# Performance work log

Measured on AMD Instinct MI355X. Metric: run time of the kernel, lower is better.

The kernel has to match this reference:

```python
import jax, jax.numpy as jnp
import numpy as np

H, KV, D, HID = 32, 2, 128, 4096
SQ, SMAX, CP, L = 1024, 4096, 3072, 4
LAYER_IDX = 0


def setup_inputs() -> dict:
    key = jax.random.key(0)
    ks = jax.random.split(key, 14)
    hidden_states = jax.random.normal(ks[0], (1, HID, 1, SQ), jnp.float32)
    # RoPE tables (values in [-1,1]; layout per forward: cos/sin act on last dim of K,
    # cos_t/sin_t are the transposed tables acting on dim -2 of Q)
    cos = jax.random.uniform(ks[1], (1, 1, SQ, D), jnp.float32, -1.0, 1.0)
    sin = jax.random.uniform(ks[2], (1, 1, SQ, D), jnp.float32, -1.0, 1.0)
    cos_t = jax.random.uniform(ks[3], (1, 1, D, SQ), jnp.float32, -1.0, 1.0)
    sin_t = jax.random.uniform(ks[4], (1, 1, D, SQ), jnp.float32, -1.0, 1.0)
    # causal mask in (kv_pos, q_pos) layout: query q sits at absolute position CP+q
    kv_pos = jnp.arange(SMAX)[:, None]
    q_pos = jnp.arange(SQ)[None, :]
    attention_mask = jnp.where(kv_pos <= CP + q_pos, 0.0, -1e9).astype(jnp.float32)[None, None]
    key_cache = jax.random.normal(ks[5], (L, KV, SMAX, D), jnp.float32)
    value_cache = jax.random.normal(ks[6], (L, KV, SMAX, D), jnp.float32)
    s = 0.02
    wq = jax.random.normal(ks[7], (H * D, HID), jnp.float32) * s
    bq = jax.random.normal(ks[8], (H * D,), jnp.float32) * s
    wk = jax.random.normal(ks[9], (KV * D, HID), jnp.float32) * s
    bk = jax.random.normal(ks[10], (KV * D,), jnp.float32) * s
    wv = jax.random.normal(ks[11], (KV * D, HID), jnp.float32) * s
    bv = jax.random.normal(ks[12], (KV * D,), jnp.float32) * s
    wo = jax.random.normal(ks[13], (HID, H * D), jnp.float32) * s
    return dict(hidden_states=hidden_states, cos=cos, sin=sin, cos_t=cos_t, sin_t=sin_t,
                attention_mask=attention_mask, key_cache=key_cache, value_cache=value_cache,
                wq=wq, bq=bq, wk=wk, bk=bk, wv=wv, bv=bv, wo=wo, cache_position=CP)


def _rotate_half(x, axis):
    x1, x2 = jnp.split(x, 2, axis=axis)
    return jnp.concatenate([-x2, x1], axis=axis)


def reference(hidden_states, cos, sin, cos_t, sin_t, attention_mask,
              key_cache, value_cache, wq, bq, wk, bk, wv, bv, wo, cache_position):
    cp = int(cache_position)
    # 1x1-conv projections == matmul over channel dim; hidden_states (1, HID, 1, SQ)
    q = jnp.einsum('oi,bihs->bohs', wq, hidden_states) + bq[None, :, None, None]
    k = jnp.einsum('oi,bihs->bohs', wk, hidden_states) + bk[None, :, None, None]
    v = jnp.einsum('oi,bihs->bohs', wv, hidden_states) + bv[None, :, None, None]
    q = q.reshape(1, H, D, SQ)                      # (1, H, D, Sq)
    k = k.reshape(1, KV, D, SQ).swapaxes(2, 3)      # (1, KV, Sq, D)
    v = v.reshape(1, KV, D, SQ).swapaxes(2, 3)      # (1, KV, Sq, D)
    # split-half RoPE: q rotated along dim -2 (head_dim axis), k along dim -1
    q = q * cos_t + _rotate_half(q, -2) * sin_t
    k = k * cos + _rotate_half(k, -1) * sin
    # scatter into KV cache at [layer_idx, :, cp:cp+SQ]
    kc = key_cache.at[LAYER_IDX, :, cp:cp + SQ, :].set(k[0])
    vc = value_cache.at[LAYER_IDX, :, cp:cp + SQ, :].set(v[0])
    kl = kc[LAYER_IDX]   # (KV, Smax, D)
    vl = vc[LAYER_IDX]   # (KV, Smax, D)
    qg = q.reshape(KV, H // KV, D, SQ)  # group G=H/KV query heads per kv head
    # K @ Q per kv-head group, softmax over kv positions (axis=2)
    attn = jnp.einsum('ksd,kgdq->kgsq', kl, qg) / jnp.sqrt(jnp.float32(D))
    attn = attn + attention_mask[0]     # broadcast (1, Smax, Sq) over (KV, G, Smax, Sq)
    attn = jax.nn.softmax(attn, axis=2)
    out = jnp.einsum('kgsq,ksd->kgqd', attn, vl)    # (KV, G, Sq, D)
    out = out.reshape(1, H, SQ, D).swapaxes(2, 3).reshape(1, H * D, 1, SQ)
    out = jnp.einsum('oi,bihs->bohs', wo, out)      # (1, HID, 1, Sq)
    return out
```

## Files before the change

kernel.cpp:

```cpp
#include <hip/hip_runtime.h>
#include <stdint.h>

#define H_    32
#define KV_   2
#define D_    128
#define HID_  4096
#define SQ_   1024
#define SMAX_ 4096

typedef unsigned short u16;
typedef __attribute__((ext_vector_type(8))) short bf16x8;
typedef __attribute__((ext_vector_type(8))) unsigned short u16x8;
typedef __attribute__((ext_vector_type(4))) float f32x4;

#define MFMA16(a, b, c) __builtin_amdgcn_mfma_f32_16x16x32_bf16(a, b, c, 0, 0, 0)

__device__ __forceinline__ u16 f2bf(float f) {
  unsigned u = __float_as_uint(f);
  u += 0x7fffu + ((u >> 16) & 1u);
  return (u16)(u >> 16);
}
__device__ __forceinline__ float bf2f(u16 u) {
  return __uint_as_float(((unsigned)u) << 16);
}
__device__ __forceinline__ float exp2_fast(float x) {
  float r;
  asm("v_exp_f32 %0, %1" : "=v"(r) : "v"(x));
  return r;
}
__device__ __forceinline__ unsigned cvt_pk_bf16(float lo, float hi) {
  unsigned r;
  asm("v_cvt_pk_bf16_f32 %0, %1, %2" : "=v"(r) : "v"(lo), "v"(hi));
  return r;
}

__device__ __forceinline__ void gl_lds16(const void* g, void* l) {
  __builtin_amdgcn_global_load_lds(
      (const __attribute__((address_space(1))) unsigned int*)g,
      (__attribute__((address_space(3))) unsigned int*)l, 16, 0, 0);
}

__global__ __launch_bounds__(256) void k_ht(const float* __restrict__ hs,
                                            u16* __restrict__ ht) {
  __shared__ float tl[64][65];
  const int i0 = blockIdx.x << 6, s0 = blockIdx.y << 6;
  const int tid = threadIdx.x;
  {
    const int r = tid >> 2, c = (tid & 3) << 4;
    const float* p = hs + (i0 + r) * SQ_ + s0 + c;
    float4 a = *(const float4*)p;
    float4 b = *(const float4*)(p + 4);
    float4 cc = *(const float4*)(p + 8);
    float4 d = *(const float4*)(p + 12);
    float* q = &tl[r][c];
    q[0] = a.x; q[1] = a.y; q[2] = a.z; q[3] = a.w;
    q[4] = b.x; q[5] = b.y; q[6] = b.z; q[7] = b.w;
    q[8] = cc.x; q[9] = cc.y; q[10] = cc.z; q[11] = cc.w;
    q[12] = d.x; q[13] = d.y; q[14] = d.z; q[15] = d.w;
  }
  __syncthreads();
  {
    const int sr = tid >> 2, c = (tid & 3) << 4;
    u16x8 o0, o1;
#pragma unroll
    for (int j = 0; j < 8; ++j) o0[j] = f2bf(tl[c + j][sr]);
#pragma unroll
    for (int j = 0; j < 8; ++j) o1[j] = f2bf(tl[c + 8 + j][sr]);
    u16* q = ht + (s0 + sr) * HID_ + i0 + c;
    *(u16x8*)q = o0;
    *(u16x8*)(q + 8) = o1;
  }
}

__global__ __launch_bounds__(256) void k_wconv4(const float* __restrict__ s0,
                                                const float* __restrict__ s1,
                                                const float* __restrict__ s2,
                                                const float* __restrict__ s3,
                                                u16* __restrict__ dbase) {
  const int N0 = (H_ * D_ * HID_) / 8;
  const int N1 = (KV_ * D_ * HID_) / 8;
  const int NT = N0 + 2 * N1 + N0;
  const int stride = gridDim.x << 8;
  for (int i = (blockIdx.x << 8) + threadIdx.x; i < NT; i += stride) {
    const float* s;
    int j;
    if (i < N0) { s = s0; j = i; }
    else if (i < N0 + N1) { s = s1; j = i - N0; }
    else if (i < N0 + 2 * N1) { s = s2; j = i - N0 - N1; }
    else { s = s3; j = i - N0 - 2 * N1; }
    const float4 a = ((const float4*)s)[2 * j];
    const float4 b = ((const float4*)s)[2 * j + 1];
    u16x8 o;
    o[0] = f2bf(a.x); o[1] = f2bf(a.y); o[2] = f2bf(a.z); o[3] = f2bf(a.w);
    o[4] = f2bf(b.x); o[5] = f2bf(b.y); o[6] = f2bf(b.z); o[7] = f2bf(b.w);
    ((u16x8*)dbase)[i] = o;
  }
}

template <int OUTMODE, bool SWZ>
__global__ __launch_bounds__(256, 2) void k_gemm_bf(const u16* __restrict__ A,
                                                    const float* __restrict__ bias,
                                                    const u16* __restrict__ B,
                                                    void* __restrict__ Cout,
                                                    const int* __restrict__ cpp,
                                                    int ldc,
                                                    const float* __restrict__ bk2,
                                                    const float* __restrict__ bv2,
                                                    u16* __restrict__ knr2,
                                                    u16* __restrict__ vt2) {
  __shared__ u16 a_t[2][64 * 64];
  __shared__ u16 b_t[2][128 * 64];
  int nx, my;
  if (SWZ) {
    const int bid = blockIdx.x;
    const int xcd = bid & 7, t = bid >> 3;
    nx = t & 7;
    my = ((t >> 3) << 3) | xcd;
  } else {
    nx = blockIdx.x;
    my = blockIdx.y;
  }
  const int n0 = nx << 7, m0 = my << 6;
  const int tid = threadIdx.x, wid = tid >> 6, lane = tid & 63;
  const int l15 = lane & 15, l4 = lane >> 4;
  const int wn = wid << 5;
  const f32x4 z4 = {0.f, 0.f, 0.f, 0.f};
  f32x4 acc[4][2];
#pragma unroll
  for (int i = 0; i < 4; ++i)
#pragma unroll
    for (int j = 0; j < 2; ++j) acc[i][j] = z4;

  const int lr8 = lane >> 3, sl = lane & 7;
  const char* sp[6];
  u16* dp[6];
  int stp[6];
#pragma unroll
  for (int j = 0; j < 6; ++j) {
    const int L = wid * 6 + j;
    const bool isA = (L < 8);
    const int Lr = isA ? L : (L - 8);
    const int row = (Lr << 3) + lr8;
    const int cs = sl ^ (row & 7);
    const size_t grow = isA ? (size_t)(m0 + row) : (size_t)(n0 + row);
    sp[j] = (const char*)((isA ? A : B) + grow * HID_) + (cs << 4);
    dp[j] = (isA ? &a_t[0][0] : &b_t[0][0]) + (Lr << 9);
    stp[j] = isA ? 4096 : 8192;
  }
#define GSTAGE(buf, kt)                                     \
  {                                                         \
    _Pragma("unroll") for (int j = 0; j < 6; ++j)           \
        gl_lds16(sp[j] + ((size_t)(kt) << 7),               \
                 dp[j] + ((buf) ? stp[j] : 0));             \
  }

  GSTAGE(0, 0);
  __syncthreads();
  int cur = 0;
  for (int kt = 0; kt < HID_ / 64; ++kt) {
    if (kt + 1 < HID_ / 64) GSTAGE(cur ^ 1, kt + 1);
#pragma unroll
    for (int kk = 0; kk < 2; ++kk) {
      bf16x8 af[4], bfr[2];
#pragma unroll
      for (int mf = 0; mf < 4; ++mf) {
        const int row = mf * 16 + l15;
        const int slt = ((kk << 2) + l4) ^ (row & 7);
        af[mf] = *(const bf16x8*)((const char*)&a_t[cur][0] + (row << 7) + (slt << 4));
      }
#pragma unroll
      for (int nf = 0; nf < 2; ++nf) {
        const int row = wn + nf * 16 + l15;
        const int slt = ((kk << 2) + l4) ^ (row & 7);
        bfr[nf] = *(const bf16x8*)((const char*)&b_t[cur][0] + (row << 7) + (slt << 4));
      }
#pragma unroll
      for (int nf = 0; nf < 2; ++nf)
#pragma unroll
        for (int mf = 0; mf < 4; ++mf) acc[mf][nf] = MFMA16(af[mf], bfr[nf], acc[mf][nf]);
    }
    __syncthreads();
    cur ^= 1;
  }
#undef GSTAGE

  if (OUTMODE == 3) {
    const int cp = cpp[0];
#pragma unroll
    for (int mf = 0; mf < 4; ++mf) {
#pragma unroll
      for (int r = 0; r < 4; ++r) {
        const int m = m0 + mf * 16 + (l4 << 2) + r;
        float bi;
        u16* dst;
        if (m < 4096) { bi = bias[m]; dst = (u16*)Cout + (size_t)m * SQ_; }
        else if (m < 4352) { bi = bk2[m - 4096]; dst = knr2 + (size_t)(m - 4096) * SQ_; }
        else { bi = bv2[m - 4352]; dst = vt2 + (size_t)(m - 4352) * SMAX_ + cp; }
#pragma unroll
        for (int nf = 0; nf < 2; ++nf) {
          const int n = n0 + wn + nf * 16 + l15;
          dst[n] = f2bf(acc[mf][nf][r] + bi);
        }
      }
    }
  } else {
#pragma unroll
    for (int mf = 0; mf < 4; ++mf) {
#pragma unroll
      for (int r = 0; r < 4; ++r) {
        const int m = m0 + mf * 16 + (l4 << 2) + r;
        const float bi = bias ? bias[m] : 0.f;
#pragma unroll
        for (int nf = 0; nf < 2; ++nf) {
          const int n = n0 + wn + nf * 16 + l15;
          const float v = acc[mf][nf][r] + bi;
          if (OUTMODE == 2)
            ((float*)Cout)[(size_t)m * ldc + n] = v;
          else
            ((u16*)Cout)[(size_t)m * ldc + n] = f2bf(v);
        }
      }
    }
  }
}

template <int OUTMODE>
__global__ __launch_bounds__(256) void k_gemm_f32A(const float* __restrict__ A,
                                                   const float* __restrict__ bias,
                                                   const u16* __restrict__ B,
                                                   void* __restrict__ Cout,
                                                   const int* __restrict__ cpp,
                                                   int ldc) {
  __shared__ u16 a_t[128 * 32];
  __shared__ u16 b_t[128 * 32];
  const int n0 = blockIdx.x << 7, m0 = blockIdx.y << 7;
  const int tid = threadIdx.x;
  const int wid = tid >> 6, lane = tid & 63;
  const int l15 = lane & 15, l4 = lane >> 4;
  const int wm = (wid >> 1) * 64, wn = (wid & 1) * 64;
  const f32x4 z4 = {0.f, 0.f, 0.f, 0.f};
  f32x4 acc[4][4];
#pragma unroll
  for (int i = 0; i < 4; ++i)
#pragma unroll
    for (int j = 0; j < 4; ++j) acc[i][j] = z4;
  const int arow = tid >> 1, ac = (tid & 1) << 4;
  const float* Ap = A + (size_t)(m0 + arow) * HID_ + ac;
  const u16* Bp = B + (size_t)(n0 + arow) * HID_ + ac;
  for (int kt = 0; kt < HID_ / 32; ++kt) {
    float4 f0 = *(const float4*)(Ap);
    float4 f1 = *(const float4*)(Ap + 4);
    float4 f2 = *(const float4*)(Ap + 8);
    float4 f3 = *(const float4*)(Ap + 12);
    uint4 b0 = *(const uint4*)(Bp);
    uint4 b1 = *(const uint4*)(Bp + 8);
    Ap += 32;
    Bp += 32;
    u16x8 ua0, ua1;
    ua0[0] = f2bf(f0.x); ua0[1] = f2bf(f0.y); ua0[2] = f2bf(f0.z); ua0[3] = f2bf(f0.w);
    ua0[4] = f2bf(f1.x); ua0[5] = f2bf(f1.y); ua0[6] = f2bf(f1.z); ua0[7] = f2bf(f1.w);
    ua1[0] = f2bf(f2.x); ua1[1] = f2bf(f2.y); ua1[2] = f2bf(f2.z); ua1[3] = f2bf(f2.w);
    ua1[4] = f2bf(f3.x); ua1[5] = f2bf(f3.y); ua1[6] = f2bf(f3.z); ua1[7] = f2bf(f3.w);
    __syncthreads();
    *(u16x8*)&a_t[arow * 32 + ac] = ua0;
    *(u16x8*)&a_t[arow * 32 + ac + 8] = ua1;
    *(uint4*)&b_t[arow * 32 + ac] = b0;
    *(uint4*)&b_t[arow * 32 + ac + 8] = b1;
    __syncthreads();
    bf16x8 af[4];
#pragma unroll
    for (int mf = 0; mf < 4; ++mf)
      af[mf] = *(const bf16x8*)&a_t[(wm + mf * 16 + l15) * 32 + l4 * 8];
#pragma unroll
    for (int nf = 0; nf < 4; ++nf) {
      bf16x8 bfr = *(const bf16x8*)&b_t[(wn + nf * 16 + l15) * 32 + l4 * 8];
#pragma unroll
      for (int mf = 0; mf < 4; ++mf) acc[mf][nf] = MFMA16(af[mf], bfr, acc[mf][nf]);
    }
  }
  const int coff = (OUTMODE == 1) ? cpp[0] : 0;
#pragma unroll
  for (int mf = 0; mf < 4; ++mf) {
#pragma unroll
    for (int r = 0; r < 4; ++r) {
      const int m = m0 + wm + mf * 16 + l4 * 4 + r;
      const float bi = bias ? bias[m] : 0.f;
#pragma unroll
      for (int nf = 0; nf < 4; ++nf) {
        const int n = n0 + wn + nf * 16 + l15;
        const float v = acc[mf][nf][r] + bi;
        if (OUTMODE == 2)
          ((float*)Cout)[(size_t)m * ldc + n] = v;
        else
          ((u16*)Cout)[(size_t)m * ldc + n + coff] = f2bf(v);
      }
    }
  }
}

__global__ __launch_bounds__(256) void k_rope_q(const u16* __restrict__ qnr,
                                                const float* __restrict__ cost,
                                                const float* __restrict__ sint,
                                                u16* __restrict__ Qr) {
  __shared__ u16 qt[128 * 64];
  __shared__ float ct[128 * 64];
  __shared__ float st[128 * 64];
  const int s0 = blockIdx.x << 6, h = blockIdx.y;
  const int tid = threadIdx.x;
  {
    const int r = tid >> 1, c = (tid & 1) << 5;
    const u16* p = qnr + (h * 128 + r) * SQ_ + s0 + c;
#pragma unroll
    for (int j = 0; j < 4; ++j) *(uint4*)&qt[r * 64 + c + j * 8] = *(const uint4*)(p + j * 8);
    const float* cpr = cost + r * SQ_ + s0 + c;
    const float* spr = sint + r * SQ_ + s0 + c;
#pragma unroll
    for (int j = 0; j < 8; ++j) {
      *(float4*)&ct[r * 64 + c + j * 4] = *(const float4*)(cpr + j * 4);
      *(float4*)&st[r * 64 + c + j * 4] = *(const float4*)(spr + j * 4);
    }
  }
  __syncthreads();
  const int sl = tid >> 2, d0 = (tid & 3) << 5;
  u16* op = Qr + (((h << 10) + s0 + sl) << 7) + d0;
#pragma unroll
  for (int g = 0; g < 4; ++g) {
    u16x8 o;
#pragma unroll
    for (int j = 0; j < 8; ++j) {
      const int d = d0 + g * 8 + j;
      const float v = bf2f(qt[d * 64 + sl]);
      const float vp = bf2f(qt[(d ^ 64) * 64 + sl]);
      const float sgn = (d < 64) ? -1.f : 1.f;
      o[j] = f2bf(v * ct[d * 64 + sl] + sgn * vp * st[d * 64 + sl]);
    }
    *(u16x8*)(op + g * 8) = o;
  }
}

__global__ __launch_bounds__(256) void k_rope_k(const u16* __restrict__ knr,
                                                const float* __restrict__ cosp,
                                                const float* __restrict__ sinp,
                                                const int* __restrict__ cpp,
                                                u16* __restrict__ kful) {
  __shared__ u16 kt_[128 * 64];
  const int s0 = blockIdx.x << 6, kk = blockIdx.y;
  const int cp = cpp[0];
  const int tid = threadIdx.x;
  {
    const int r = tid >> 1, c = (tid & 1) << 5;
    const u16* p = knr + (kk * 128 + r) * SQ_ + s0 + c;
#pragma unroll
    for (int j = 0; j < 4; ++j) *(uint4*)&kt_[r * 64 + c + j * 8] = *(const uint4*)(p + j * 8);
  }
  __syncthreads();
  const int sl = tid >> 2, d0 = (tid & 3) << 5;
  const int s = s0 + sl;
  const float* crow = cosp + s * D_;
  const float* srow = sinp + s * D_;
  u16* op = kful + ((kk * SMAX_ + cp + s) << 7) + d0;
#pragma unroll
  for (int g = 0; g < 4; ++g) {
    u16x8 o;
#pragma unroll
    for (int j = 0; j < 8; ++j) {
      const int d = d0 + g * 8 + j;
      const float v = bf2f(kt_[d * 64 + sl]);
      const float vp = bf2f(kt_[(d ^ 64) * 64 + sl]);
      const float sgn = (d < 64) ? -1.f : 1.f;
      o[j] = f2bf(v * crow[d] + sgn * vp * srow[d]);
    }
    *(u16x8*)(op + g * 8) = o;
  }
}

__global__ __launch_bounds__(256) void k_prefk(const float* __restrict__ kc,
                                               const int* __restrict__ cpp,
                                               u16* __restrict__ kful) {
  const int cp = cpp[0];
  const int idx = (blockIdx.x << 8) + threadIdx.x;
  const int base = idx << 3;
  const int s = (base >> 7) & (SMAX_ - 1);
  if (s >= cp) return;
  const float* p = kc + base;
  float4 a = *(const float4*)p;
  float4 b = *(const float4*)(p + 4);
  u16x8 o;
  o[0] = f2bf(a.x); o[1] = f2bf(a.y); o[2] = f2bf(a.z); o[3] = f2bf(a.w);
  o[4] = f2bf(b.x); o[5] = f2bf(b.y); o[6] = f2bf(b.z); o[7] = f2bf(b.w);
  *(u16x8*)(kful + base) = o;
}

__global__ __launch_bounds__(256) void k_prefvt(const float* __restrict__ vc,
                                                const int* __restrict__ cpp,
                                                u16* __restrict__ vt) {
  const int cp = cpp[0];
  const int s0 = blockIdx.x << 6, d0 = blockIdx.y << 6, kk = blockIdx.z;
  if (s0 >= cp) return;
  __shared__ float tl[64][65];
  const int tid = threadIdx.x;
  {
    const int r = tid >> 2, c = (tid & 3) << 4;
    if (s0 + r < cp) {
      const float* p = vc + ((kk * SMAX_ + s0 + r) << 7) + d0 + c;
#pragma unroll
      for (int j = 0; j < 4; ++j) {
        float4 v = *(const float4*)(p + j * 4);
        tl[r][c + j * 4 + 0] = v.x;
        tl[r][c + j * 4 + 1] = v.y;
        tl[r][c + j * 4 + 2] = v.z;
        tl[r][c + j * 4 + 3] = v.w;
      }
    }
  }
  __syncthreads();
  const int dl = tid >> 2, c = (tid & 3) << 4;
  u16* op = vt + (kk * D_ + d0 + dl) * SMAX_ + s0 + c;
  if (s0 + c + 15 < cp) {
    u16x8 o0, o1;
#pragma unroll
    for (int j = 0; j < 8; ++j) o0[j] = f2bf(tl[c + j][dl]);
#pragma unroll
    for (int j = 0; j < 8; ++j) o1[j] = f2bf(tl[c + 8 + j][dl]);
    *(u16x8*)op = o0;
    *(u16x8*)(op + 8) = o1;
  } else {
#pragma unroll
    for (int j = 0; j < 16; ++j)
      if (s0 + c + j < cp) op[j] = f2bf(tl[c + j][dl]);
  }
}

__device__ __forceinline__ void attn_stageK8(const char* KfB, int kv0, u16* kbuf,
                                             int wid, int lane) {
  const int kcb = (lane & 15) << 4;
#pragma unroll
  for (int j = 0; j < 2; ++j) {
    const int L = (wid << 1) + j;
    const int row = (L << 2) + (lane >> 4);
    gl_lds16(KfB + (((size_t)(kv0 + row)) << 8) + (kcb ^ ((row & 7) << 4)),
             kbuf + (L << 9));
  }
}
__device__ __forceinline__ void attn_stageV8(const char* VtB, int kv0, u16* vbuf,
                                             int wid, int lane) {
  const int vcb = (lane & 7) << 4;
#pragma unroll
  for (int j = 0; j < 2; ++j) {
    const int L = (wid << 1) + j;
    const int row = (L << 3) + (lane >> 3);
    gl_lds16(VtB + ((((size_t)row * SMAX_) + kv0) << 1) + (vcb ^ ((row & 7) << 4)),
             vbuf + (L << 9));
  }
}

template <int SPLIT>
__global__ __launch_bounds__(512, 4) void k_attn(const u16* __restrict__ Q,
                                                 const u16* __restrict__ Kf,
                                                 const u16* __restrict__ Vt,
                                                 const int* __restrict__ cpp,
                                                 u16* __restrict__ Ob,
                                                 float* __restrict__ Opart,
                                                 float* __restrict__ Ml) {
  __shared__ u16 Kb[2][8192];
  __shared__ u16 Vb[2][8192];
  __shared__ u16 Pl[8][1024];
  int h, qb, ch;
  if (SPLIT) {
    const int bid = blockIdx.x;
    const int xcd = bid & 7, s = bid >> 3;
    h = ((xcd >> 2) << 4) | (xcd & 3) | ((s & 3) << 2);
    qb = (s >> 2) & 7;
    ch = s >> 5;
  } else {
    h = blockIdx.x;
    qb = blockIdx.y;
    ch = 0;
  }
  const int cp = cpp[0];
  const int kk = h >> 4;
  const int tid = threadIdx.x, wid = tid >> 6, lane = tid & 63;
  const int l15 = lane & 15, l4 = lane >> 4;
  const int qrow_base = (qb << 7) + (wid << 4);
  char* pl = (char*)&Pl[wid][0];

  bf16x8 aq[4];
#pragma unroll
  for (int ks = 0; ks < 4; ++ks)
    aq[ks] = *(const bf16x8*)&Q[(((size_t)(h << 10) + qrow_base + l15) << 7) + ks * 32 + (l4 << 3)];

  const f32x4 z4 = {0.f, 0.f, 0.f, 0.f};
  f32x4 oacc[8];
  float mrun = -1e30f, lrun = 0.f;
#pragma unroll
  for (int nf = 0; nf < 8; ++nf) oacc[nf] = z4;

  const int ntf0 = ((cp + (qb << 7) + 127) >> 6) + 1;
  const int ntf = ntf0 < (SMAX_ >> 6) ? ntf0 : (SMAX_ >> 6);
  const int t0 = (SPLIT && ch) ? 32 : 0;
  const int t1 = (SPLIT && !ch) ? 32 : ntf;
  const float SC2 = 0.12751879523568785f;

  const char* KfB = (const char*)Kf + ((size_t)kk * SMAX_ << 8);
  const char* VtB = (const char*)Vt + ((size_t)kk << 20);

  attn_stageK8(KfB, t0 << 6, Kb[0], wid, lane);
  attn_stageV8(VtB, t0 << 6, Vb[0], wid, lane);
  __syncthreads();
  int cur = 0;

  for (int kt = t0; kt < t1; ++kt) {
    const int kv0 = kt << 6;
    if (kt + 1 < t1) {
      attn_stageK8(KfB, kv0 + 64, Kb[cur ^ 1], wid, lane);
      attn_stageV8(VtB, kv0 + 64, Vb[cur ^ 1], wid, lane);
    }
    const char* kb = (const char*)Kb[cur];
    const char* vb = (const char*)Vb[cur];
    f32x4 sa[4];
#pragma unroll
    for (int nf = 0; nf < 4; ++nf) sa[nf] = z4;
#pragma unroll
    for (int ks = 0; ks < 4; ++ks) {
#pragma unroll
      for (int nf = 0; nf < 4; ++nf) {
        const int rk = nf * 16 + l15;
        bf16x8 bk = *(const bf16x8*)(kb + (((rk << 8) + (ks << 6) + (l4 << 4)) ^ ((rk & 7) << 4)));
        sa[nf] = MFMA16(bk, aq[ks], sa[nf]);
      }
    }
    const int lim = cp + qrow_base + l15;
    if ((kv0 + 63) > (cp + qrow_base)) {
#pragma unroll
      for (int nf = 0; nf < 4; ++nf)
#pragma unroll
        for (int r = 0; r < 4; ++r)
          if (kv0 + nf * 16 + (l4 << 2) + r > lim) sa[nf][r] = -8e9f;
    }
    float t4[4];
#pragma unroll
    for (int nf = 0; nf < 4; ++nf)
      t4[nf] = fmaxf(fmaxf(sa[nf][0], sa[nf][1]), fmaxf(sa[nf][2], sa[nf][3]));
    float ml = fmaxf(fmaxf(t4[0], t4[1]), fmaxf(t4[2], t4[3])) * SC2;
    ml = fmaxf(ml, __shfl_xor(ml, 16));
    ml = fmaxf(ml, __shfl_xor(ml, 32));
    const bool need = !__all(ml <= mrun + 11.54f);
    const float mnew = need ? fmaxf(ml, mrun) : mrun;
    const float nm = -mnew;
    float rs = 0.f;
#pragma unroll
    for (int nf = 0; nf < 4; ++nf) {
      const float p0 = exp2_fast(fmaf(sa[nf][0], SC2, nm));
      const float p1 = exp2_fast(fmaf(sa[nf][1], SC2, nm));
      const float p2 = exp2_fast(fmaf(sa[nf][2], SC2, nm));
      const float p3 = exp2_fast(fmaf(sa[nf][3], SC2, nm));
      rs += (p0 + p1) + (p2 + p3);
      uint2 w;
      w.x = cvt_pk_bf16(p0, p1);
      w.y = cvt_pk_bf16(p2, p3);
      const unsigned byte = (unsigned)(((l15 << 7) + (nf << 5) + (l4 << 3)) ^ ((l15 & 7) << 4));
      *(uint2*)(pl + byte) = w;
    }
    rs += __shfl_xor(rs, 16);
    rs += __shfl_xor(rs, 32);
    if (need) {
      const float sf = exp2_fast(mrun - mnew);
      lrun = lrun * sf + rs;
      mrun = mnew;
      float sfr[4];
#pragma unroll
      for (int r = 0; r < 4; ++r) sfr[r] = __shfl(sf, (l4 << 2) + r);
#pragma unroll
      for (int nf = 0; nf < 8; ++nf)
#pragma unroll
        for (int r = 0; r < 4; ++r) oacc[nf][r] *= sfr[r];
    } else {
      lrun += rs;
    }
    bf16x8 ap[2];
#pragma unroll
    for (int k2 = 0; k2 < 2; ++k2) {
      const unsigned byte = (unsigned)(((l15 << 7) + (k2 << 6) + (l4 << 4)) ^ ((l15 & 7) << 4));
      ap[k2] = *(const bf16x8*)(pl + byte);
    }
#pragma unroll
    for (int nf = 0; nf < 8; ++nf) {
#pragma unroll
      for (int k2 = 0; k2 < 2; ++k2) {
        const int rv = nf * 16 + l15;
        bf16x8 bv = *(const bf16x8*)(vb + (((rv << 7) + (k2 << 6) + (l4 << 4)) ^ ((rv & 7) << 4)));
        oacc[nf] = MFMA16(ap[k2], bv, oacc[nf]);
      }
    }
    __syncthreads();
    cur ^= 1;
  }

  float lq[4], mq[4];
#pragma unroll
  for (int r = 0; r < 4; ++r) {
    lq[r] = __shfl(lrun, (l4 << 2) + r);
    mq[r] = __shfl(mrun, (l4 << 2) + r);
  }
  if (SPLIT) {
    float* Obase = Opart + ((((size_t)ch << 5) + h) << 17);
#pragma unroll
    for (int r = 0; r < 4; ++r) {
      const int row = qrow_base + (l4 << 2) + r;
      float* op = Obase + ((size_t)row << 7);
#pragma unroll
      for (int nf = 0; nf < 8; ++nf) op[nf * 16 + l15] = oacc[nf][r];
      if (l15 == 0) {
        float* mlp = Ml + ((((((size_t)ch << 5) + h) << 10) + row) << 1);
        mlp[0] = mq[r];
        mlp[1] = lq[r];
      }
    }
  } else {
#pragma unroll
    for (int r = 0; r < 4; ++r) {
      const float inv = 1.f / lq[r];
      const int qrow = qrow_base + (l4 << 2) + r;
#pragma unroll
      for (int nf = 0; nf < 8; ++nf)
        Ob[((size_t)qrow << 12) + (h << 7) + nf * 16 + l15] = f2bf(oacc[nf][r] * inv);
    }
  }
}

__global__ __launch_bounds__(256) void k_merge(const float* __restrict__ Opart,
                                               const float* __restrict__ Ml,
                                               u16* __restrict__ Ob) {
  const int h = blockIdx.x, qb = blockIdx.y;
  const int tid = threadIdx.x;
  const int row = (qb << 6) + (tid >> 2);
  const int d0 = (tid & 3) << 5;
  const size_t r0 = ((size_t)h << 10) + row;
  const size_t r1 = r0 + ((size_t)32 << 10);
  const float m0 = Ml[2 * r0], l0 = Ml[2 * r0 + 1];
  const float m1 = Ml[2 * r1], l1 = Ml[2 * r1 + 1];
  const float mm = fmaxf(m0, m1);
  const float w0 = exp2_fast(m0 - mm), w1 = exp2_fast(m1 - mm);
  const float inv = 1.f / (w0 * l0 + w1 * l1);
  const float a0 = w0 * inv, a1 = w1 * inv;
  const float* p0 = Opart + (r0 << 7) + d0;
  const float* p1 = Opart + (r1 << 7) + d0;
  u16* ob = Ob + (((size_t)row) << 12) + (h << 7) + d0;
#pragma unroll
  for (int g = 0; g < 4; ++g) {
    float4 u = *(const float4*)(p0 + g * 8);
    float4 v = *(const float4*)(p0 + g * 8 + 4);
    float4 x = *(const float4*)(p1 + g * 8);
    float4 y = *(const float4*)(p1 + g * 8 + 4);
    u16x8 o;
    o[0] = f2bf(a0 * u.x + a1 * x.x);
    o[1] = f2bf(a0 * u.y + a1 * x.y);
    o[2] = f2bf(a0 * u.z + a1 * x.z);
    o[3] = f2bf(a0 * u.w + a1 * x.w);
    o[4] = f2bf(a0 * v.x + a1 * y.x);
    o[5] = f2bf(a0 * v.y + a1 * y.y);
    o[6] = f2bf(a0 * v.z + a1 * y.z);
    o[7] = f2bf(a0 * v.w + a1 * y.w);
    *(u16x8*)(ob + g * 8) = o;
  }
}

extern "C" void kernel_launch(void* const* d_in, const int* in_sizes, int n_in,
                              void* d_out, int out_size, void* d_ws, size_t ws_size,
                              hipStream_t stream) {
  const float* hs    = (const float*)d_in[0];
  const float* cosp  = (const float*)d_in[1];
  const float* sinp  = (const float*)d_in[2];
  const float* cost  = (const float*)d_in[3];
  const float* sint  = (const float*)d_in[4];
  const float* kcache = (const float*)d_in[6];
  const float* vcache = (const float*)d_in[7];
  const float* wq = (const float*)d_in[8];
  const float* bq = (const float*)d_in[9];
  const float* wk = (const float*)d_in[10];
  const float* bk = (const float*)d_in[11];
  const float* wv = (const float*)d_in[12];
  const float* bv = (const float*)d_in[13];
  const float* wo = (const float*)d_in[14];
  const int* cpp = (const int*)d_in[15];

  char* ws = (char*)d_ws;
  u16* ht   = (u16*)(ws);
  u16* qnr  = (u16*)(ws + 8388608);
  u16* Qr   = (u16*)(ws + 16777216);
  u16* knr  = (u16*)(ws + 25165824);
  u16* kful = (u16*)(ws + 25690112);
  u16* vt   = (u16*)(ws + 27787264);
  u16* Ob   = (u16*)(ws + 29884416);

  const size_t WOFF  = 38273024;
  const size_t SZ_WQ = (size_t)H_ * D_ * HID_ * 2;
  const size_t SZ_WK = (size_t)KV_ * D_ * HID_ * 2;
  const size_t SZ_WO = (size_t)HID_ * H_ * D_ * 2;
  const size_t OPOFF = WOFF + SZ_WQ + 2 * SZ_WK + SZ_WO;
  const size_t SZ_OP = (size_t)2 * 32 * 1024 * 128 * 4;
  const size_t MLOFF = OPOFF + SZ_OP;
  const size_t SZ_ML = (size_t)2 * 32 * 1024 * 2 * 4;
  const bool pre = ws_size >= OPOFF;
  const bool splitok = pre && ws_size >= MLOFF + SZ_ML;

  k_ht<<<dim3(64, 16), 256, 0, stream>>>(hs, ht);
  if (pre) {
    u16* wqb = (u16*)(ws + WOFF);
    u16* wkb = (u16*)(ws + WOFF + SZ_WQ);
    u16* wvb = (u16*)(ws + WOFF + SZ_WQ + SZ_WK);
    u16* wob = (u16*)(ws + WOFF + SZ_WQ + 2 * SZ_WK);
    float* Opart = (float*)(ws + OPOFF);
    float* Ml    = (float*)(ws + MLOFF);
    k_wconv4<<<2048, 256, 0, stream>>>(wq, wk, wv, wo, wqb);
    k_gemm_bf<3, true><<<576, 256, 0, stream>>>(wqb, bq, ht, (void*)qnr, cpp, SQ_,
                                                bk, bv, knr, vt);
    k_rope_q<<<dim3(16, 32), 256, 0, stream>>>(qnr, cost, sint, Qr);
    k_rope_k<<<dim3(16, 2), 256, 0, stream>>>(knr, cosp, sinp, cpp, kful);
    k_prefk<<<dim3(512), 256, 0, stream>>>(kcache, cpp, kful);
    k_prefvt<<<dim3(64, 2, 2), 256, 0, stream>>>(vcache, cpp, vt);
    if (splitok) {
      k_attn<1><<<512, 512, 0, stream>>>(Qr, kful, vt, cpp, Ob, Opart, Ml);
      k_merge<<<dim3(32, 16), 256, 0, stream>>>(Opart, Ml, Ob);
    } else {
      k_attn<0><<<dim3(32, 8), 512, 0, stream>>>(Qr, kful, vt, cpp, Ob, nullptr, nullptr);
    }
    k_gemm_bf<2, true><<<512, 256, 0, stream>>>(wob, nullptr, Ob, d_out, nullptr, SQ_,
                                                nullptr, nullptr, nullptr, nullptr);
  } else {
    k_gemm_f32A<0><<<dim3(8, 32), 256, 0, stream>>>(wq, bq, ht, (void*)qnr, nullptr, SQ_);
    k_gemm_f32A<0><<<dim3(8, 2), 256, 0, stream>>>(wk, bk, ht, (void*)knr, nullptr, SQ_);
    k_gemm_f32A<1><<<dim3(8, 2), 256, 0, stream>>>(wv, bv, ht, (void*)vt, cpp, SMAX_);
    k_rope_q<<<dim3(16, 32), 256, 0, stream>>>(qnr, cost, sint, Qr);
    k_rope_k<<<dim3(16, 2), 256, 0, stream>>>(knr, cosp, sinp, cpp, kful);
    k_prefk<<<dim3(512), 256, 0, stream>>>(kcache, cpp, kful);
    k_prefvt<<<dim3(64, 2, 2), 256, 0, stream>>>(vcache, cpp, vt);
    k_attn<0><<<dim3(32, 8), 512, 0, stream>>>(Qr, kful, vt, cpp, Ob, nullptr, nullptr);
    k_gemm_f32A<2><<<dim3(8, 32), 256, 0, stream>>>(wo, nullptr, Ob, d_out, nullptr, SQ_);
  }
  (void)in_sizes; (void)n_in; (void)out_size; (void)ws_size;
}
```

Before: 278.7 us.

## Process two 16-row query groups per wave in attention to reuse K/V fragments

The attention kernel now runs 4 waves (256 threads) per block instead of 8. Each wave handles 32 query rows as two 16-row groups, so every K and V fragment read from LDS feeds two MFMAs, halving LDS reads per MFMA. Staging loops load twice as many rows per wave to keep the same 64-row K/V tiles. In exchange each wave holds roughly twice the accumulator registers, and there are fewer waves per block to hide latency.

Result: faster. 267.7 us (-4.0%).

```diff
diff --git a/kernel.cpp b/kernel.cpp
--- a/kernel.cpp
+++ b/kernel.cpp
@@ -431,31 +431,80 @@
   }
 }
 
-__device__ __forceinline__ void attn_stageK8(const char* KfB, int kv0, u16* kbuf,
+__device__ __forceinline__ void attn_stageK4(const char* KfB, int kv0, u16* kbuf,
                                              int wid, int lane) {
   const int kcb = (lane & 15) << 4;
 #pragma unroll
-  for (int j = 0; j < 2; ++j) {
-    const int L = (wid << 1) + j;
+  for (int j = 0; j < 4; ++j) {
+    const int L = (wid << 2) + j;
     const int row = (L << 2) + (lane >> 4);
     gl_lds16(KfB + (((size_t)(kv0 + row)) << 8) + (kcb ^ ((row & 7) << 4)),
              kbuf + (L << 9));
   }
 }
-__device__ __forceinline__ void attn_stageV8(const char* VtB, int kv0, u16* vbuf,
+__device__ __forceinline__ void attn_stageV4(const char* VtB, int kv0, u16* vbuf,
                                              int wid, int lane) {
   const int vcb = (lane & 7) << 4;
 #pragma unroll
-  for (int j = 0; j < 2; ++j) {
-    const int L = (wid << 1) + j;
+  for (int j = 0; j < 4; ++j) {
+    const int L = (wid << 2) + j;
     const int row = (L << 3) + (lane >> 3);
     gl_lds16(VtB + ((((size_t)row * SMAX_) + kv0) << 1) + (vcb ^ ((row & 7) << 4)),
              vbuf + (L << 9));
   }
 }
 
+#define SOFTMAX_G(g, sarr)                                               \
+  {                                                                      \
+    const int lim = cp + qrow_base + (g << 4) + l15;                     \
+    if ((kv0 + 63) > (cp + qrow_base + (g << 4))) {                      \
+      _Pragma("unroll") for (int nf = 0; nf < 4; ++nf)                   \
+          _Pragma("unroll") for (int r = 0; r < 4; ++r)                  \
+          if (kv0 + nf * 16 + (l4 << 2) + r > lim) sarr[nf][r] = -8e9f;  \
+    }                                                                    \
+    float t4[4];                                                         \
+    _Pragma("unroll") for (int nf = 0; nf < 4; ++nf)                     \
+        t4[nf] = fmaxf(fmaxf(sarr[nf][0], sarr[nf][1]),                  \
+                       fmaxf(sarr[nf][2], sarr[nf][3]));                 \
+    float ml = fmaxf(fmaxf(t4[0], t4[1]), fmaxf(t4[2], t4[3])) * SC2;    \
+    ml = fmaxf(ml, __shfl_xor(ml, 16));                                  \
+    ml = fmaxf(ml, __shfl_xor(ml, 32));                                  \
+    const bool need = !__all(ml <= mrun[g] + 11.54f);                    \
+    const float mnew = need ? fmaxf(ml, mrun[g]) : mrun[g];              \
+    const float nm = -mnew;                                              \
+    float rs = 0.f;                                                      \
+    _Pragma("unroll") for (int nf = 0; nf < 4; ++nf) {                   \
+      const float p0 = exp2_fast(fmaf(sarr[nf][0], SC2, nm));            \
+      const float p1 = exp2_fast(fmaf(sarr[nf][1], SC2, nm));            \
+      const float p2 = exp2_fast(fmaf(sarr[nf][2], SC2, nm));            \
+      const float p3 = exp2_fast(fmaf(sarr[nf][3], SC2, nm));            \
+      rs += (p0 + p1) + (p2 + p3);                                       \
+      uint2 w;                                                           \
+      w.x = cvt_pk_bf16(p0, p1);                                         \
+      w.y = cvt_pk_bf16(p2, p3);                                         \
+      const unsigned byte = (unsigned)(((((g << 4) + l15) << 7) +        \
+          (nf << 5) + (l4 << 3)) ^ ((l15 & 7) << 4));                    \
+      *(uint2*)(pl + byte) = w;                                          \
+    }                                                                    \
+    rs += __shfl_xor(rs, 16);                                            \
+    rs += __shfl_xor(rs, 32);                                            \
+    if (need) {                                                          \
+      const float sf = exp2_fast(mrun[g] - mnew);                        \
+      lrun[g] = lrun[g] * sf + rs;                                       \
+      mrun[g] = mnew;                                                    \
+      float sfr[4];                                                      \
+      _Pragma("unroll") for (int r = 0; r < 4; ++r)                      \
+          sfr[r] = __shfl(sf, (l4 << 2) + r);                            \
+      _Pragma("unroll") for (int nf = 0; nf < 8; ++nf)                   \
+          _Pragma("unroll") for (int r = 0; r < 4; ++r)                  \
+          oacc[g][nf][r] *= sfr[r];                                      \
+    } else {                                                             \
+      lrun[g] += rs;                                                     \
+    }                                                                    \
+  }
+
 template <int SPLIT>
-__global__ __launch_bounds__(512, 4) void k_attn(const u16* __restrict__ Q,
+__global__ __launch_bounds__(256, 2) void k_attn(const u16* __restrict__ Q,
                                                  const u16* __restrict__ Kf,
                                                  const u16* __restrict__ Vt,
                                                  const int* __restrict__ cpp,
@@ -464,7 +513,7 @@
                                                  float* __restrict__ Ml) {
   __shared__ u16 Kb[2][8192];
   __shared__ u16 Vb[2][8192];
-  __shared__ u16 Pl[8][1024];
+  __shared__ u16 Pl[4][2048];
   int h, qb, ch;
   if (SPLIT) {
     const int bid = blockIdx.x;
@@ -481,19 +530,27 @@
   const int kk = h >> 4;
   const int tid = threadIdx.x, wid = tid >> 6, lane = tid & 63;
   const int l15 = lane & 15, l4 = lane >> 4;
-  const int qrow_base = (qb << 7) + (wid << 4);
+  const int qrow_base = (qb << 7) + (wid << 5);
   char* pl = (char*)&Pl[wid][0];
 
-  bf16x8 aq[4];
-#pragma unroll
-  for (int ks = 0; ks < 4; ++ks)
-    aq[ks] = *(const bf16x8*)&Q[(((size_t)(h << 10) + qrow_base + l15) << 7) + ks * 32 + (l4 << 3)];
+  bf16x8 aq[2][4];
+#pragma unroll
+  for (int g = 0; g < 2; ++g)
+#pragma unroll
+    for (int ks = 0; ks < 4; ++ks)
+      aq[g][ks] = *(const bf16x8*)&Q[(((size_t)(h << 10) + qrow_base + (g << 4) + l15) << 7) +
+                                     ks * 32 + (l4 << 3)];
 
   const f32x4 z4 = {0.f, 0.f, 0.f, 0.f};
-  f32x4 oacc[8];
-  float mrun = -1e30f, lrun = 0.f;
-#pragma unroll
-  for (int nf = 0; nf < 8; ++nf) oacc[nf] = z4;
+  f32x4 oacc[2][8];
+  float mrun[2], lrun[2];
+#pragma unroll
+  for (int g = 0; g < 2; ++g) {
+#pragma unroll
+    for (int nf = 0; nf < 8; ++nf) oacc[g][nf] = z4;
+    mrun[g] = -1e30f;
+    lrun[g] = 0.f;
+  }
 
   const int ntf0 = ((cp + (qb << 7) + 127) >> 6) + 1;
   const int ntf = ntf0 < (SMAX_ >> 6) ? ntf0 : (SMAX_ >> 6);
@@ -504,127 +561,92 @@
   const char* KfB = (const char*)Kf + ((size_t)kk * SMAX_ << 8);
   const char* VtB = (const char*)Vt + ((size_t)kk << 20);
 
-  attn_stageK8(KfB, t0 << 6, Kb[0], wid, lane);
-  attn_stageV8(VtB, t0 << 6, Vb[0], wid, lane);
+  attn_stageK4(KfB, t0 << 6, Kb[0], wid, lane);
+  attn_stageV4(VtB, t0 << 6, Vb[0], wid, lane);
   __syncthreads();
   int cur = 0;
 
   for (int kt = t0; kt < t1; ++kt) {
     const int kv0 = kt << 6;
     if (kt + 1 < t1) {
-      attn_stageK8(KfB, kv0 + 64, Kb[cur ^ 1], wid, lane);
-      attn_stageV8(VtB, kv0 + 64, Vb[cur ^ 1], wid, lane);
+      attn_stageK4(KfB, kv0 + 64, Kb[cur ^ 1], wid, lane);
+      attn_stageV4(VtB, kv0 + 64, Vb[cur ^ 1], wid, lane);
     }
     const char* kb = (const char*)Kb[cur];
     const char* vb = (const char*)Vb[cur];
-    f32x4 sa[4];
-#pragma unroll
-    for (int nf = 0; nf < 4; ++nf) sa[nf] = z4;
+    f32x4 s0[4], s1[4];
+#pragma unroll
+    for (int nf = 0; nf < 4; ++nf) { s0[nf] = z4; s1[nf] = z4; }
 #pragma unroll
     for (int ks = 0; ks < 4; ++ks) {
 #pragma unroll
       for (int nf = 0; nf < 4; ++nf) {
         const int rk = nf * 16 + l15;
         bf16x8 bk = *(const bf16x8*)(kb + (((rk << 8) + (ks << 6) + (l4 << 4)) ^ ((rk & 7) << 4)));
-        sa[nf] = MFMA16(bk, aq[ks], sa[nf]);
-      }
-    }
-    const int lim = cp + qrow_base + l15;
-    if ((kv0 + 63) > (cp + qrow_base)) {
-#pragma unroll
-      for (int nf = 0; nf < 4; ++nf)
-#pragma unroll
-        for (int r = 0; r < 4; ++r)
-          if (kv0 + nf * 16 + (l4 << 2) + r > lim) sa[nf][r] = -8e9f;
-    }
-    float t4[4];
-#pragma unroll
-    for (int nf = 0; nf < 4; ++nf)
-      t4[nf] = fmaxf(fmaxf(sa[nf][0], sa[nf][1]), fmaxf(sa[nf][2], sa[nf][3]));
-    float ml = fmaxf(fmaxf(t4[0], t4[1]), fmaxf(t4[2], t4[3])) * SC2;
-    ml = fmaxf(ml, __shfl_xor(ml, 16));
-    ml = fmaxf(ml, __shfl_xor(ml, 32));
-    const bool need = !__all(ml <= mrun + 11.54f);
-    const float mnew = need ? fmaxf(ml, mrun) : mrun;
-    const float nm = -mnew;
-    float rs = 0.f;
-#pragma unroll
-    for (int nf = 0; nf < 4; ++nf) {
-      const float p0 = exp2_fast(fmaf(sa[nf][0], SC2, nm));
-      const float p1 = exp2_fast(fmaf(sa[nf][1], SC2, nm));
-      const float p2 = exp2_fast(fmaf(sa[nf][2], SC2, nm));
-      const float p3 = exp2_fast(fmaf(sa[nf][3], SC2, nm));
-      rs += (p0 + p1) + (p2 + p3);
-      uint2 w;
-      w.x = cvt_pk_bf16(p0, p1);
-      w.y = cvt_pk_bf16(p2, p3);
-      const unsigned byte = (unsigned)(((l15 << 7) + (nf << 5) + (l4 << 3)) ^ ((l15 & 7) << 4));
-      *(uint2*)(pl + byte) = w;
-    }
-    rs += __shfl_xor(rs, 16);
-    rs += __shfl_xor(rs, 32);
-    if (need) {
-      const float sf = exp2_fast(mrun - mnew);
-      lrun = lrun * sf + rs;
-      mrun = mnew;
-      float sfr[4];
-#pragma unroll
-      for (int r = 0; r < 4; ++r) sfr[r] = __shfl(sf, (l4 << 2) + r);
-#pragma unroll
-      for (int nf = 0; nf < 8; ++nf)
-#pragma unroll
-        for (int r = 0; r < 4; ++r) oacc[nf][r] *= sfr[r];
-    } else {
-      lrun += rs;
-    }
-    bf16x8 ap[2];
-#pragma unroll
-    for (int k2 = 0; k2 < 2; ++k2) {
-      const unsigned byte = (unsigned)(((l15 << 7) + (k2 << 6) + (l4 << 4)) ^ ((l15 & 7) << 4));
-      ap[k2] = *(const bf16x8*)(pl + byte);
-    }
+        s0[nf] = MFMA16(bk, aq[0][ks], s0[nf]);
+        s1[nf] = MFMA16(bk, aq[1][ks], s1[nf]);
+      }
+    }
+    SOFTMAX_G(0, s0)
+    SOFTMAX_G(1, s1)
+    bf16x8 ap[2][2];
+#pragma unroll
+    for (int g = 0; g < 2; ++g)
+#pragma unroll
+      for (int k2 = 0; k2 < 2; ++k2) {
+        const unsigned byte = (unsigned)(((((g << 4) + l15) << 7) + (k2 << 6) + (l4 << 4)) ^
+                                         ((l15 & 7) << 4));
+        ap[g][k2] = *(const bf16x8*)(pl + byte);
+      }
 #pragma unroll
     for (int nf = 0; nf < 8; ++nf) {
 #pragma unroll
       for (int k2 = 0; k2 < 2; ++k2) {
         const int rv = nf * 16 + l15;
         bf16x8 bv = *(const bf16x8*)(vb + (((rv << 7) + (k2 << 6) + (l4 << 4)) ^ ((rv & 7) << 4)));
-        oacc[nf] = MFMA16(ap[k2], bv, oacc[nf]);
+        oacc[0][nf] = MFMA16(ap[0][k2], bv, oacc[0][nf]);
+        oacc[1][nf] = MFMA16(ap[1][k2], bv, oacc[1][nf]);
       }
     }
     __syncthreads();
     cur ^= 1;
   }
 
-  float lq[4], mq[4];
-#pragma unroll
-  for (int r = 0; r < 4; ++r) {
-    lq[r] = __shfl(lrun, (l4 << 2) + r);
-    mq[r] = __shfl(mrun, (l4 << 2) + r);
-  }
+  float lq[2][4], mq[2][4];
+#pragma unroll
+  for (int g = 0; g < 2; ++g)
+#pragma unroll
+    for (int r = 0; r < 4; ++r) {
+      lq[g][r] = __shfl(lrun[g], (l4 << 2) + r);
+      mq[g][r] = __shfl(mrun[g], (l4 << 2) + r);
+    }
   if (SPLIT) {
     float* Obase = Opart + ((((size_t)ch << 5) + h) << 17);
 #pragma unroll
-    for (int r = 0; r < 4; ++r) {
-      const int row = qrow_base + (l4 << 2) + r;
-      float* op = Obase + ((size_t)row << 7);
-#pragma unroll
-      for (int nf = 0; nf < 8; ++nf) op[nf * 16 + l15] = oacc[nf][r];
-      if (l15 == 0) {
-        float* mlp = Ml + ((((((size_t)ch << 5) + h) << 10) + row) << 1);
-        mlp[0] = mq[r];
-        mlp[1] = lq[r];
-      }
-    }
+    for (int g = 0; g < 2; ++g)
+#pragma unroll
+      for (int r = 0; r < 4; ++r) {
+        const int row = qrow_base + (g << 4) + (l4 << 2) + r;
+        float* op = Obase + ((size_t)row << 7);
+#pragma unroll
+        for (int nf = 0; nf < 8; ++nf) op[nf * 16 + l15] = oacc[g][nf][r];
+        if (l15 == 0) {
+          float* mlp = Ml + ((((((size_t)ch << 5) + h) << 10) + row) << 1);
+          mlp[0] = mq[g][r];
+          mlp[1] = lq[g][r];
+        }
+      }
   } else {
 #pragma unroll
-    for (int r = 0; r < 4; ++r) {
-      const float inv = 1.f / lq[r];
-      const int qrow = qrow_base + (l4 << 2) + r;
-#pragma unroll
-      for (int nf = 0; nf < 8; ++nf)
-        Ob[((size_t)qrow << 12) + (h << 7) + nf * 16 + l15] = f2bf(oacc[nf][r] * inv);
-    }
+    for (int g = 0; g < 2; ++g)
+#pragma unroll
+      for (int r = 0; r < 4; ++r) {
+        const float inv = 1.f / lq[g][r];
+        const int qrow = qrow_base + (g << 4) + (l4 << 2) + r;
+#pragma unroll
+        for (int nf = 0; nf < 8; ++nf)
+          Ob[((size_t)qrow << 12) + (h << 7) + nf * 16 + l15] = f2bf(oacc[g][nf][r] * inv);
+      }
   }
 }
 
@@ -720,10 +742,10 @@
     k_prefk<<<dim3(512), 256, 0, stream>>>(kcache, cpp, kful);
     k_prefvt<<<dim3(64, 2, 2), 256, 0, stream>>>(vcache, cpp, vt);
     if (splitok) {
-      k_attn<1><<<512, 512, 0, stream>>>(Qr, kful, vt, cpp, Ob, Opart, Ml);
+      k_attn<1><<<512, 256, 0, stream>>>(Qr, kful, vt, cpp, Ob, Opart, Ml);
       k_merge<<<dim3(32, 16), 256, 0, stream>>>(Opart, Ml, Ob);
     } else {
-      k_attn<0><<<dim3(32, 8), 512, 0, stream>>>(Qr, kful, vt, cpp, Ob, nullptr, nullptr);
+      k_attn<0><<<dim3(32, 8), 256, 0, stream>>>(Qr, kful, vt, cpp, Ob, nullptr, nullptr);
     }
     k_gemm_bf<2, true><<<512, 256, 0, stream>>>(wob, nullptr, Ob, d_out, nullptr, SQ_,
                                                 nullptr, nullptr, nullptr, nullptr);
@@ -735,7 +757,7 @@
     k_rope_k<<<dim3(16, 2), 256, 0, stream>>>(knr, cosp, sinp, cpp, kful);
     k_prefk<<<dim3(512), 256, 0, stream>>>(kcache, cpp, kful);
     k_prefvt<<<dim3(64, 2, 2), 256, 0, stream>>>(vcache, cpp, vt);
-    k_attn<0><<<dim3(32, 8), 512, 0, stream>>>(Qr, kful, vt, cpp, Ob, nullptr, nullptr);
+    k_attn<0><<<dim3(32, 8), 256, 0, stream>>>(Qr, kful, vt, cpp, Ob, nullptr, nullptr);
     k_gemm_f32A<2><<<dim3(8, 32), 256, 0, stream>>>(wo, nullptr, Ob, d_out, nullptr, SQ_);
   }
   (void)in_sizes; (void)n_in; (void)out_size; (void)ws_size;
```
